# Kernel optimization log

Measured on AMD Instinct MI355X. Metric: run time of the kernel, lower is better.

Reference implementation:

```python
import jax, jax.numpy as jnp
import numpy as np


def _deform_conv2d(x, offset, weight, stride=(1, 1), pad=(1, 1), dilation=(1, 1)):
    # x: [B,C,H,W]; offset: [B, 2*Goff*kh*kw, oh, ow]; weight: [OC, C//Gw, kh, kw]
    B, C, H, W = x.shape
    OC, Cg, kh, kw = weight.shape
    Gw = C // Cg
    K = kh * kw
    sh, sw = stride
    ph, pw = pad
    dh, dw = dilation
    oh = (H + 2 * ph - (dh * (kh - 1) + 1)) // sh + 1
    ow = (W + 2 * pw - (dw * (kw - 1) + 1)) // sw + 1
    Goff = offset.shape[1] // (2 * K)
    # torchvision layout: per offset group, per kernel tap k, (dy, dx)
    off = offset.reshape(B, Goff, K, 2, oh, ow)
    ki = jnp.arange(K) // kw  # kernel row per tap
    kj = jnp.arange(K) % kw   # kernel col per tap
    base_y = jnp.arange(oh) * sh - ph
    base_x = jnp.arange(ow) * sw - pw
    gy = (base_y[None, :] + (ki * dh)[:, None]).astype(x.dtype)  # [K, oh]
    gx = (base_x[None, :] + (kj * dw)[:, None]).astype(x.dtype)  # [K, ow]
    py = off[:, :, :, 0] + gy[None, None, :, :, None]  # [B,Goff,K,oh,ow]
    px = off[:, :, :, 1] + gx[None, None, :, None, :]
    cpg = C // Goff  # channels per offset group
    py = jnp.repeat(py, cpg, axis=1)  # [B,C,K,oh,ow]
    px = jnp.repeat(px, cpg, axis=1)
    xf = x.reshape(B, C, H * W)
    y0 = jnp.floor(py)
    x0 = jnp.floor(px)
    ty = py - y0
    tx = px - x0
    y0i = y0.astype(jnp.int32)
    x0i = x0.astype(jnp.int32)

    def gather(cy, cx):
        valid = (cy >= 0) & (cy < H) & (cx >= 0) & (cx < W)
        idx = jnp.clip(cy, 0, H - 1) * W + jnp.clip(cx, 0, W - 1)
        v = jnp.take_along_axis(xf, idx.reshape(B, C, -1), axis=2).reshape(idx.shape)
        return jnp.where(valid, v, jnp.zeros((), x.dtype))

    # bilinear sample, zero padding outside image (matches torchvision)
    v = (gather(y0i, x0i) * (1 - ty) * (1 - tx)
         + gather(y0i, x0i + 1) * (1 - ty) * tx
         + gather(y0i + 1, x0i) * ty * (1 - tx)
         + gather(y0i + 1, x0i + 1) * ty * tx)  # [B,C,K,oh,ow]
    v = v.reshape(B, Gw, Cg, K, oh, ow)
    wg = weight.reshape(Gw, OC // Gw, Cg, K)
    out = jnp.einsum('bgckhw,gock->bgohw', v, wg)
    return out.reshape(B, OC, oh, ow)


def setup_inputs() -> dict:
    key = jax.random.key(0)
    k1, k2, k3 = jax.random.split(key, 3)
    x = jax.random.normal(k1, (8, 64, 56, 56), dtype=jnp.float32)
    offset = jax.random.normal(k2, (8, 18, 56, 56), dtype=jnp.float32)
    weight = jax.random.normal(k3, (64, 64, 3, 3), dtype=jnp.float32) * 0.05
    return {"input": x, "offset": offset, "weight": weight}


def reference(input, offset, weight):
    return _deform_conv2d(input, offset, weight, stride=(1, 1), pad=(1, 1), dilation=(1, 1))
```

## Files before the change

### kernel.cpp

```cpp
#include <hip/hip_runtime.h>
#include <hip/hip_fp16.h>


typedef _Float16 f16x8 __attribute__((ext_vector_type(8)));
typedef float    f32x4 __attribute__((ext_vector_type(4)));

namespace {
constexpr int Bn = 8, Cn = 64, Hn = 56, Wn = 56;
constexpr int Kk = 9, OCn = 64;
constexpr int NPIX = 56 * 56;
constexpr int CK   = Cn * Kk;
constexpr int TP   = 32;
constexpr int TXW  = 7;
constexpr int TILES = 98;
constexpr int XTILES = NPIX / 64;
constexpr int KSTEPS = CK / 32;
}

__device__ __forceinline__ __half2 u2h(unsigned u) {
    union { unsigned u; __half2 h; } x; x.u = u; return x.h;
}
__device__ __forceinline__ unsigned bcast_h(float f) {
    unsigned short hs = __half_as_ushort(__float2half(f));
    return (unsigned)hs * 0x10001u;
}
__device__ __forceinline__ void lds_barrier() {
    asm volatile("s_waitcnt lgkmcnt(0)" ::: "memory");
    __builtin_amdgcn_s_barrier();
}
__device__ __forceinline__ void gld16(uint4& d, const unsigned short* p) {
    asm volatile("global_load_dwordx4 %0, %1, off" : "=&v"(d) : "v"(p) : "memory");
}

__global__ __launch_bounds__(256) void prep_kernel(
    const float* __restrict__ x, const float* __restrict__ w,
    unsigned short* __restrict__ xh, unsigned short* __restrict__ wh2)
{
    const int tid = threadIdx.x;
    if (blockIdx.x >= 392) {
        const int i = (blockIdx.x - 392) * 256 + tid;
        if (i < OCn * CK) {
            const int j    = i & 7;
            const int lane = (i >> 3) & 63;
            const int rest = i >> 9;
            const int og   = rest / KSTEPS;
            const int oc   = og * 16 + (lane & 15);
            const int kglob = (rest % KSTEPS) * 32 + (lane >> 4) * 8 + j;
            const int tap = kglob >> 6;
            const int c   = kglob & 63;
            wh2[i] = __half_as_ushort(__float2half(w[oc * CK + c * Kk + tap]));
        }
        return;
    }
    __shared__ unsigned short lds[64][66];
    const int b  = blockIdx.x & 7;
    const int t0 = (blockIdx.x >> 3) * 64;
    const float* xb = x + (size_t)b * Cn * NPIX;
    {
        const int hw0 = (tid & 15) * 4;
        #pragma unroll
        for (int i = 0; i < 4; ++i) {
            const int c = (tid >> 4) + i * 16;
            const float4 v = *(const float4*)(xb + (size_t)c * NPIX + t0 + hw0);
            lds[hw0 + 0][c] = __half_as_ushort(__float2half(v.x));
            lds[hw0 + 1][c] = __half_as_ushort(__float2half(v.y));
            lds[hw0 + 2][c] = __half_as_ushort(__float2half(v.z));
            lds[hw0 + 3][c] = __half_as_ushort(__float2half(v.w));
        }
    }
    __syncthreads();
    {
        const int co = (tid & 7) * 8;
        #pragma unroll
        for (int i = 0; i < 2; ++i) {
            const int hw = (tid >> 3) + i * 32;
            unsigned short tmp[8] __attribute__((aligned(16)));
            #pragma unroll
            for (int j = 0; j < 8; ++j) tmp[j] = lds[hw][co + j];
            *(uint4*)(xh + ((size_t)b * NPIX + t0 + hw) * Cn + co) = *(const uint4*)tmp;
        }
    }
}

__global__ __launch_bounds__(256, 3) void deform_fused(
    const unsigned short* __restrict__ xh, const float* __restrict__ off,
    const unsigned short* __restrict__ wh2, float* __restrict__ out)
{
    __shared__ uint4 smpw[Kk * TP];
    __shared__ int4  smpa[Kk * TP];
    __shared__ __align__(16) uint4 vbuf[3][8 * TP];

    const int tid = threadIdx.x;
    const int b   = blockIdx.x & 7;
    const int t   = blockIdx.x >> 3;
    const int ox0 = (t % TXW) * 8;
    const int oy0 = (t / TXW) * 4;
    const unsigned short* xb = xh + (size_t)b * NPIX * Cn;
    const float* offb = off + (size_t)b * 18 * NPIX;

    for (int e = tid; e < Kk * TP; e += 256) {
        const int k  = e >> 5;
        const int px = e & 31;
        const int oy = oy0 + (px >> 3);
        const int ox = ox0 + (px & 7);
        const int p  = oy * Wn + ox;
        const int ki = k / 3, kj = k % 3;
        const float offy = offb[(size_t)(2 * k)     * NPIX + p];
        const float offx = offb[(size_t)(2 * k + 1) * NPIX + p];
        const float py  = offy + (float)(oy - 1 + ki);
        const float pxv = offx + (float)(ox - 1 + kj);
        const float y0f = floorf(py), x0f = floorf(pxv);
        const float ty = py - y0f, tx = pxv - x0f;
        const int y0 = (int)y0f, x0 = (int)x0f;
        const int y1 = y0 + 1, x1 = x0 + 1;
        const bool vy0 = (y0 >= 0) & (y0 < Hn);
        const bool vy1 = (y1 >= 0) & (y1 < Hn);
        const bool vx0 = (x0 >= 0) & (x0 < Wn);
        const bool vx1 = (x1 >= 0) & (x1 < Wn);
        const int cy0 = min(max(y0, 0), Hn - 1);
        const int cy1 = min(max(y1, 0), Hn - 1);
        const int cx0 = min(max(x0, 0), Wn - 1);
        const int cx1 = min(max(x1, 0), Wn - 1);
        uint4 wq;
        wq.x = bcast_h((vy0 && vx0) ? (1.f - ty) * (1.f - tx) : 0.f);
        wq.y = bcast_h((vy0 && vx1) ? (1.f - ty) * tx         : 0.f);
        wq.z = bcast_h((vy1 && vx0) ? ty * (1.f - tx)         : 0.f);
        wq.w = bcast_h((vy1 && vx1) ? ty * tx                 : 0.f);
        int4 av;
        av.x = (cy0 * Wn + cx0) * Cn;
        av.y = (cy0 * Wn + cx1) * Cn;
        av.z = (cy1 * Wn + cx0) * Cn;
        av.w = (cy1 * Wn + cx1) * Cn;
        smpw[e] = wq;
        smpa[e] = av;
    }
    lds_barrier();
    asm volatile("s_waitcnt vmcnt(0)" ::: "memory");

    const int oct = tid & 7;
    const int gpx = (tid >> 3) & 31;
    const int co  = oct * 8;

    const int lane = tid & 63;
    const int og   = tid >> 6;
    const int hi   = lane >> 4;
    const int lr   = lane & 15;
    const uint4* ab = (const uint4*)wh2 + (size_t)og * KSTEPS * 64 + lane;

    uint4 s0[2], s1[2], s2[2], s3[2], wqr[2];
    uint4 aF[2][2];
    f32x4 acc0 = {0.f, 0.f, 0.f, 0.f};
    f32x4 acc1 = {0.f, 0.f, 0.f, 0.f};

    auto stageC = [&](int k) {
        const int sl = k & 1;
        const int m  = k * TP + gpx;
        const int4 av = smpa[m];
        wqr[sl] = smpw[m];
        gld16(s0[sl], xb + av.x + co);
        gld16(s1[sl], xb + av.y + co);
        gld16(s2[sl], xb + av.z + co);
        gld16(s3[sl], xb + av.w + co);
    };
    auto loadA = [&](int k) {
        const int sl = k & 1;
        gld16(aF[sl][0], (const unsigned short*)(ab + (k * 2 + 0) * 64));
        gld16(aF[sl][1], (const unsigned short*)(ab + (k * 2 + 1) * 64));
    };
    auto blend = [&](int k) {
        const int sl = k & 1;
        const __half2 w00 = u2h(wqr[sl].x), w01 = u2h(wqr[sl].y);
        const __half2 w10 = u2h(wqr[sl].z), w11 = u2h(wqr[sl].w);
        uint4 res;
        unsigned* rp = (unsigned*)&res;
        #pragma unroll
        for (int q = 0; q < 4; ++q) {
            __half2 a = __hmul2(w00, u2h(((const unsigned*)&s0[sl])[q]));
            a = __hfma2(w01, u2h(((const unsigned*)&s1[sl])[q]), a);
            a = __hfma2(w10, u2h(((const unsigned*)&s2[sl])[q]), a);
            a = __hfma2(w11, u2h(((const unsigned*)&s3[sl])[q]), a);
            rp[q] = *(const unsigned*)&a;
        }
        vbuf[k % 3][oct * TP + gpx] = res;
    };
    auto mfma = [&](int k) {
        const int sl = k % 3;
        #pragma unroll
        for (int kl = 0; kl < 2; ++kl) {
            const int octr = kl * 4 + hi;
            union { uint4 u; f16x8 h; } a, b0, b1;
            a.u  = aF[k & 1][kl];
            b0.u = vbuf[sl][octr * TP + lr];
            b1.u = vbuf[sl][octr * TP + 16 + lr];
            acc0 = __builtin_amdgcn_mfma_f32_16x16x32_f16(a.h, b0.h, acc0, 0, 0, 0);
            acc1 = __builtin_amdgcn_mfma_f32_16x16x32_f16(a.h, b1.h, acc1, 0, 0, 0);
        }
    };

    stageC(0); stageC(1);
    loadA(0);
    asm volatile("s_waitcnt vmcnt(6)" ::: "memory");
    __builtin_amdgcn_sched_barrier(0);
    blend(0);
    lds_barrier();

    #pragma unroll
    for (int k = 0; k < Kk; ++k) {
        if (k < Kk - 2) stageC(k + 2);
        if (k < Kk - 1) loadA(k + 1);
        if (k < Kk - 2)      asm volatile("s_waitcnt vmcnt(6)" ::: "memory");
        else if (k == Kk - 2) asm volatile("s_waitcnt vmcnt(2)" ::: "memory");
        else                  asm volatile("s_waitcnt vmcnt(0)" ::: "memory");
        __builtin_amdgcn_sched_barrier(0);
        if (k < Kk - 1) blend(k + 1);
        mfma(k);
        lds_barrier();
    }

    const int p_lo = (oy0 + (lr >> 3)) * Wn + ox0 + (lr & 7);
    const int p_hi = (oy0 + 2 + (lr >> 3)) * Wn + ox0 + (lr & 7);
    float* ob = out + ((size_t)b * OCn + og * 16 + hi * 4) * NPIX;
    #pragma unroll
    for (int r = 0; r < 4; ++r) {
        ob[(size_t)r * NPIX + p_lo] = acc0[r];
        ob[(size_t)r * NPIX + p_hi] = acc1[r];
    }
}

extern "C" void kernel_launch(void* const* d_in, const int* in_sizes, int n_in,
                              void* d_out, int out_size, void* d_ws, size_t ws_size,
                              hipStream_t stream) {
    const float* x   = (const float*)d_in[0];
    const float* off = (const float*)d_in[1];
    const float* w   = (const float*)d_in[2];
    float* out = (float*)d_out;
    unsigned short* wh2 = (unsigned short*)d_ws;
    unsigned short* xh  = (unsigned short*)((char*)d_ws + 131072);

    hipLaunchKernelGGL(prep_kernel, dim3(392 + 144), dim3(256), 0, stream, x, w, xh, wh2);
    hipLaunchKernelGGL(deform_fused, dim3(Bn * TILES), dim3(256), 0, stream,
                       xh, off, wh2, out);
}
```

Before: 20.46 us.

## Stage input neighbourhood window in LDS and sample bilinear taps from shared memory

Each block first loads a 13x17-pixel, 64-channel fp16 window of the input around its 4x8 output tile into LDS. Bilinear corner samples whose coordinates fall inside the window are read from LDS, and those outside fall back to global loads. The hand-scheduled two-stage global-load pipeline with explicit vmcnt waits is replaced by a simpler blend-then-MFMA loop with a double-buffered vbuf. This cuts scattered global gathers but adds about 56KB of LDS per block, which may limit occupancy, and drops the overlap of gather latency with MFMA work.

```diff
diff --git a/kernel.cpp b/kernel.cpp
--- a/kernel.cpp
+++ b/kernel.cpp
@@ -15,6 +15,9 @@
 constexpr int TILES = 98;
 constexpr int XTILES = NPIX / 64;
 constexpr int KSTEPS = CK / 32;
+constexpr int WR = 13, WC = 17;
+constexpr int WSITES = WR * WC;
+constexpr int WU4 = WSITES * 8;
 }
 
 __device__ __forceinline__ __half2 u2h(unsigned u) {
@@ -27,9 +30,6 @@
 __device__ __forceinline__ void lds_barrier() {
     asm volatile("s_waitcnt lgkmcnt(0)" ::: "memory");
     __builtin_amdgcn_s_barrier();
-}
-__device__ __forceinline__ void gld16(uint4& d, const unsigned short* p) {
-    asm volatile("global_load_dwordx4 %0, %1, off" : "=&v"(d) : "v"(p) : "memory");
 }
 
 __global__ __launch_bounds__(256) void prep_kernel(
@@ -88,15 +88,30 @@
 {
     __shared__ uint4 smpw[Kk * TP];
     __shared__ int4  smpa[Kk * TP];
-    __shared__ __align__(16) uint4 vbuf[3][8 * TP];
+    __shared__ int4  smpl[Kk * TP];
+    __shared__ __align__(16) uint4 win[WU4];
+    __shared__ __align__(16) uint4 vbuf[2][8 * TP];
 
     const int tid = threadIdx.x;
     const int b   = blockIdx.x & 7;
     const int t   = blockIdx.x >> 3;
     const int ox0 = (t % TXW) * 8;
     const int oy0 = (t / TXW) * 4;
+    const int r0  = min(max(oy0 - 4, 0), Hn - WR);
+    const int c0  = min(max(ox0 - 4, 0), Wn - WC);
     const unsigned short* xb = xh + (size_t)b * NPIX * Cn;
     const float* offb = off + (size_t)b * 18 * NPIX;
+
+    uint4 st[7];
+    #pragma unroll
+    for (int it = 0; it < 7; ++it) {
+        const int u = tid + 256 * it;
+        if (u < WU4) {
+            const int i   = u / 136;
+            const int rem = u - i * 136;
+            st[it] = *(const uint4*)(xb + ((size_t)((r0 + i) * Wn + c0)) * Cn + rem * 8);
+        }
+    }
 
     for (int e = tid; e < Kk * TP; e += 256) {
         const int k  = e >> 5;
@@ -131,15 +146,28 @@
         av.y = (cy0 * Wn + cx1) * Cn;
         av.z = (cy1 * Wn + cx0) * Cn;
         av.w = (cy1 * Wn + cx1) * Cn;
+        const int i00y = cy0 - r0, i00x = cx0 - c0;
+        const int i11y = cy1 - r0, i11x = cx1 - c0;
+        int4 wl;
+        wl.x = ((unsigned)i00y < WR && (unsigned)i00x < WC) ? (i00y * WC + i00x) * 8 : -1;
+        wl.y = ((unsigned)i00y < WR && (unsigned)i11x < WC) ? (i00y * WC + i11x) * 8 : -1;
+        wl.z = ((unsigned)i11y < WR && (unsigned)i00x < WC) ? (i11y * WC + i00x) * 8 : -1;
+        wl.w = ((unsigned)i11y < WR && (unsigned)i11x < WC) ? (i11y * WC + i11x) * 8 : -1;
         smpw[e] = wq;
         smpa[e] = av;
-    }
-    lds_barrier();
-    asm volatile("s_waitcnt vmcnt(0)" ::: "memory");
+        smpl[e] = wl;
+    }
+
+    #pragma unroll
+    for (int it = 0; it < 7; ++it) {
+        const int u = tid + 256 * it;
+        if (u < WU4) win[u] = st[it];
+    }
+    __syncthreads();
 
     const int oct = tid & 7;
     const int gpx = (tid >> 3) & 31;
-    const int co  = oct * 8;
+    const int co8 = oct * 8;
 
     const int lane = tid & 63;
     const int og   = tid >> 6;
@@ -147,74 +175,61 @@
     const int lr   = lane & 15;
     const uint4* ab = (const uint4*)wh2 + (size_t)og * KSTEPS * 64 + lane;
 
-    uint4 s0[2], s1[2], s2[2], s3[2], wqr[2];
     uint4 aF[2][2];
     f32x4 acc0 = {0.f, 0.f, 0.f, 0.f};
     f32x4 acc1 = {0.f, 0.f, 0.f, 0.f};
 
-    auto stageC = [&](int k) {
-        const int sl = k & 1;
-        const int m  = k * TP + gpx;
-        const int4 av = smpa[m];
-        wqr[sl] = smpw[m];
-        gld16(s0[sl], xb + av.x + co);
-        gld16(s1[sl], xb + av.y + co);
-        gld16(s2[sl], xb + av.z + co);
-        gld16(s3[sl], xb + av.w + co);
-    };
     auto loadA = [&](int k) {
-        const int sl = k & 1;
-        gld16(aF[sl][0], (const unsigned short*)(ab + (k * 2 + 0) * 64));
-        gld16(aF[sl][1], (const unsigned short*)(ab + (k * 2 + 1) * 64));
+        aF[k & 1][0] = ab[(k * 2 + 0) * 64];
+        aF[k & 1][1] = ab[(k * 2 + 1) * 64];
     };
     auto blend = [&](int k) {
-        const int sl = k & 1;
-        const __half2 w00 = u2h(wqr[sl].x), w01 = u2h(wqr[sl].y);
-        const __half2 w10 = u2h(wqr[sl].z), w11 = u2h(wqr[sl].w);
+        const int m = k * TP + gpx;
+        const uint4 wq = smpw[m];
+        const int4  av = smpa[m];
+        const int4  wl = smpl[m];
+        uint4 v0 = win[(wl.x < 0 ? 0 : wl.x) + oct];
+        uint4 v1 = win[(wl.y < 0 ? 0 : wl.y) + oct];
+        uint4 v2 = win[(wl.z < 0 ? 0 : wl.z) + oct];
+        uint4 v3 = win[(wl.w < 0 ? 0 : wl.w) + oct];
+        if (wl.x < 0) v0 = *(const uint4*)(xb + av.x + co8);
+        if (wl.y < 0) v1 = *(const uint4*)(xb + av.y + co8);
+        if (wl.z < 0) v2 = *(const uint4*)(xb + av.z + co8);
+        if (wl.w < 0) v3 = *(const uint4*)(xb + av.w + co8);
+        const __half2 w00 = u2h(wq.x), w01 = u2h(wq.y);
+        const __half2 w10 = u2h(wq.z), w11 = u2h(wq.w);
         uint4 res;
         unsigned* rp = (unsigned*)&res;
         #pragma unroll
         for (int q = 0; q < 4; ++q) {
-            __half2 a = __hmul2(w00, u2h(((const unsigned*)&s0[sl])[q]));
-            a = __hfma2(w01, u2h(((const unsigned*)&s1[sl])[q]), a);
-            a = __hfma2(w10, u2h(((const unsigned*)&s2[sl])[q]), a);
-            a = __hfma2(w11, u2h(((const unsigned*)&s3[sl])[q]), a);
+            __half2 a = __hmul2(w00, u2h(((const unsigned*)&v0)[q]));
+            a = __hfma2(w01, u2h(((const unsigned*)&v1)[q]), a);
+            a = __hfma2(w10, u2h(((const unsigned*)&v2)[q]), a);
+            a = __hfma2(w11, u2h(((const unsigned*)&v3)[q]), a);
             rp[q] = *(const unsigned*)&a;
         }
-        vbuf[k % 3][oct * TP + gpx] = res;
+        vbuf[k & 1][oct * TP + gpx] = res;
     };
     auto mfma = [&](int k) {
-        const int sl = k % 3;
         #pragma unroll
         for (int kl = 0; kl < 2; ++kl) {
             const int octr = kl * 4 + hi;
             union { uint4 u; f16x8 h; } a, b0, b1;
             a.u  = aF[k & 1][kl];
-            b0.u = vbuf[sl][octr * TP + lr];
-            b1.u = vbuf[sl][octr * TP + 16 + lr];
+            b0.u = vbuf[k & 1][octr * TP + lr];
+            b1.u = vbuf[k & 1][octr * TP + 16 + lr];
             acc0 = __builtin_amdgcn_mfma_f32_16x16x32_f16(a.h, b0.h, acc0, 0, 0, 0);
             acc1 = __builtin_amdgcn_mfma_f32_16x16x32_f16(a.h, b1.h, acc1, 0, 0, 0);
         }
     };
 
-    stageC(0); stageC(1);
     loadA(0);
-    asm volatile("s_waitcnt vmcnt(6)" ::: "memory");
-    __builtin_amdgcn_sched_barrier(0);
-    blend(0);
-    lds_barrier();
-
     #pragma unroll
     for (int k = 0; k < Kk; ++k) {
-        if (k < Kk - 2) stageC(k + 2);
         if (k < Kk - 1) loadA(k + 1);
-        if (k < Kk - 2)      asm volatile("s_waitcnt vmcnt(6)" ::: "memory");
-        else if (k == Kk - 2) asm volatile("s_waitcnt vmcnt(2)" ::: "memory");
-        else                  asm volatile("s_waitcnt vmcnt(0)" ::: "memory");
-        __builtin_amdgcn_sched_barrier(0);
-        if (k < Kk - 1) blend(k + 1);
+        blend(k);
+        lds_barrier();
         mfma(k);
-        lds_barrier();
     }
 
     const int p_lo = (oy0 + (lr >> 3)) * Wn + ox0 + (lr & 7);
```

After: 31.23 us. +52.6%, slower.

## Warp-specialize deform kernel into gather/blend producer and MFMA consumer waves

Applied to the files above, without the earlier changes.

Splits the fused kernel into 6 waves per block: 2 producer waves gather the bilinear corner samples and blend them into the LDS ring buffer, and 4 consumer waves load weights and run MFMAs. The aim is to overlap gather latency with matrix work instead of having every wave do both serially. The cost is fewer waves doing the gathers (each handles two pixels), a larger block size that may lower occupancy under launch bounds, and barrier-coupled handoff between the roles.

```diff
diff --git a/kernel.cpp b/kernel.cpp
--- a/kernel.cpp
+++ b/kernel.cpp
@@ -15,6 +15,7 @@
 constexpr int TILES = 98;
 constexpr int XTILES = NPIX / 64;
 constexpr int KSTEPS = CK / 32;
+constexpr int NTHR = 384;
 }
 
 __device__ __forceinline__ __half2 u2h(unsigned u) {
@@ -82,7 +83,7 @@
     }
 }
 
-__global__ __launch_bounds__(256, 3) void deform_fused(
+__global__ __launch_bounds__(NTHR, 3) void deform_fused(
     const unsigned short* __restrict__ xh, const float* __restrict__ off,
     const unsigned short* __restrict__ wh2, float* __restrict__ out)
 {
@@ -98,7 +99,7 @@
     const unsigned short* xb = xh + (size_t)b * NPIX * Cn;
     const float* offb = off + (size_t)b * 18 * NPIX;
 
-    for (int e = tid; e < Kk * TP; e += 256) {
+    for (int e = tid; e < Kk * TP; e += NTHR) {
         const int k  = e >> 5;
         const int px = e & 31;
         const int oy = oy0 + (px >> 3);
@@ -137,93 +138,118 @@
     lds_barrier();
     asm volatile("s_waitcnt vmcnt(0)" ::: "memory");
 
-    const int oct = tid & 7;
-    const int gpx = (tid >> 3) & 31;
-    const int co  = oct * 8;
-
-    const int lane = tid & 63;
-    const int og   = tid >> 6;
-    const int hi   = lane >> 4;
-    const int lr   = lane & 15;
-    const uint4* ab = (const uint4*)wh2 + (size_t)og * KSTEPS * 64 + lane;
-
-    uint4 s0[2], s1[2], s2[2], s3[2], wqr[2];
-    uint4 aF[2][2];
-    f32x4 acc0 = {0.f, 0.f, 0.f, 0.f};
-    f32x4 acc1 = {0.f, 0.f, 0.f, 0.f};
-
-    auto stageC = [&](int k) {
-        const int sl = k & 1;
-        const int m  = k * TP + gpx;
-        const int4 av = smpa[m];
-        wqr[sl] = smpw[m];
-        gld16(s0[sl], xb + av.x + co);
-        gld16(s1[sl], xb + av.y + co);
-        gld16(s2[sl], xb + av.z + co);
-        gld16(s3[sl], xb + av.w + co);
-    };
-    auto loadA = [&](int k) {
-        const int sl = k & 1;
-        gld16(aF[sl][0], (const unsigned short*)(ab + (k * 2 + 0) * 64));
-        gld16(aF[sl][1], (const unsigned short*)(ab + (k * 2 + 1) * 64));
-    };
-    auto blend = [&](int k) {
-        const int sl = k & 1;
-        const __half2 w00 = u2h(wqr[sl].x), w01 = u2h(wqr[sl].y);
-        const __half2 w10 = u2h(wqr[sl].z), w11 = u2h(wqr[sl].w);
-        uint4 res;
-        unsigned* rp = (unsigned*)&res;
-        #pragma unroll
-        for (int q = 0; q < 4; ++q) {
-            __half2 a = __hmul2(w00, u2h(((const unsigned*)&s0[sl])[q]));
-            a = __hfma2(w01, u2h(((const unsigned*)&s1[sl])[q]), a);
-            a = __hfma2(w10, u2h(((const unsigned*)&s2[sl])[q]), a);
-            a = __hfma2(w11, u2h(((const unsigned*)&s3[sl])[q]), a);
-            rp[q] = *(const unsigned*)&a;
-        }
-        vbuf[k % 3][oct * TP + gpx] = res;
-    };
-    auto mfma = [&](int k) {
-        const int sl = k % 3;
-        #pragma unroll
-        for (int kl = 0; kl < 2; ++kl) {
-            const int octr = kl * 4 + hi;
-            union { uint4 u; f16x8 h; } a, b0, b1;
-            a.u  = aF[k & 1][kl];
-            b0.u = vbuf[sl][octr * TP + lr];
-            b1.u = vbuf[sl][octr * TP + 16 + lr];
-            acc0 = __builtin_amdgcn_mfma_f32_16x16x32_f16(a.h, b0.h, acc0, 0, 0, 0);
-            acc1 = __builtin_amdgcn_mfma_f32_16x16x32_f16(a.h, b1.h, acc1, 0, 0, 0);
-        }
-    };
-
-    stageC(0); stageC(1);
-    loadA(0);
-    asm volatile("s_waitcnt vmcnt(6)" ::: "memory");
-    __builtin_amdgcn_sched_barrier(0);
-    blend(0);
-    lds_barrier();
-
-    #pragma unroll
-    for (int k = 0; k < Kk; ++k) {
-        if (k < Kk - 2) stageC(k + 2);
-        if (k < Kk - 1) loadA(k + 1);
-        if (k < Kk - 2)      asm volatile("s_waitcnt vmcnt(6)" ::: "memory");
-        else if (k == Kk - 2) asm volatile("s_waitcnt vmcnt(2)" ::: "memory");
-        else                  asm volatile("s_waitcnt vmcnt(0)" ::: "memory");
+    const int wv = tid >> 6;
+
+    if (wv < 2) {
+        const int oct  = tid & 7;
+        const int gpx0 = (tid >> 3) & 15;
+        const int co   = oct * 8;
+
+        uint4 s0[2][2], s1[2][2], s2[2][2], s3[2][2], wqr[2][2];
+
+        auto stageC = [&](int k) {
+            const int sl = k & 1;
+            #pragma unroll
+            for (int u = 0; u < 2; ++u) {
+                const int m  = k * TP + gpx0 + u * 16;
+                const int4 av = smpa[m];
+                wqr[sl][u] = smpw[m];
+                gld16(s0[sl][u], xb + av.x + co);
+                gld16(s1[sl][u], xb + av.y + co);
+                gld16(s2[sl][u], xb + av.z + co);
+                gld16(s3[sl][u], xb + av.w + co);
+            }
+        };
+        auto blend = [&](int k) {
+            const int sl = k & 1;
+            #pragma unroll
+            for (int u = 0; u < 2; ++u) {
+                const __half2 w00 = u2h(wqr[sl][u].x), w01 = u2h(wqr[sl][u].y);
+                const __half2 w10 = u2h(wqr[sl][u].z), w11 = u2h(wqr[sl][u].w);
+                uint4 res;
+                unsigned* rp = (unsigned*)&res;
+                #pragma unroll
+                for (int q = 0; q < 4; ++q) {
+                    __half2 a = __hmul2(w00, u2h(((const unsigned*)&s0[sl][u])[q]));
+                    a = __hfma2(w01, u2h(((const unsigned*)&s1[sl][u])[q]), a);
+                    a = __hfma2(w10, u2h(((const unsigned*)&s2[sl][u])[q]), a);
+                    a = __hfma2(w11, u2h(((const unsigned*)&s3[sl][u])[q]), a);
+                    rp[q] = *(const unsigned*)&a;
+                }
+                vbuf[k % 3][oct * TP + gpx0 + u * 16] = res;
+            }
+        };
+
+        stageC(0); stageC(1);
+        asm volatile("s_waitcnt vmcnt(8)" ::: "memory");
         __builtin_amdgcn_sched_barrier(0);
-        if (k < Kk - 1) blend(k + 1);
-        mfma(k);
+        blend(0);
         lds_barrier();
-    }
-
-    const int p_lo = (oy0 + (lr >> 3)) * Wn + ox0 + (lr & 7);
-    const int p_hi = (oy0 + 2 + (lr >> 3)) * Wn + ox0 + (lr & 7);
-    float* ob = out + ((size_t)b * OCn + og * 16 + hi * 4) * NPIX;
-    #pragma unroll
-    for (int r = 0; r < 4; ++r) {
-        ob[(size_t)r * NPIX + p_lo] = acc0[r];
-        ob[(size_t)r * NPIX + p_hi] = acc1[r];
+
+        #pragma unroll
+        for (int k = 0; k < Kk; ++k) {
+            if (k < Kk - 2) {
+                stageC(k + 2);
+                asm volatile("s_waitcnt vmcnt(8)" ::: "memory");
+            } else if (k == Kk - 2) {
+                asm volatile("s_waitcnt vmcnt(0)" ::: "memory");
+            }
+            __builtin_amdgcn_sched_barrier(0);
+            if (k < Kk - 1) blend(k + 1);
+            lds_barrier();
+        }
+    } else {
+        const int lane = tid & 63;
+        const int og   = wv - 2;
+        const int hi   = lane >> 4;
+        const int lr   = lane & 15;
+        const uint4* ab = (const uint4*)wh2 + (size_t)og * KSTEPS * 64 + lane;
+
+        uint4 aF[2][2];
+        f32x4 acc0 = {0.f, 0.f, 0.f, 0.f};
+        f32x4 acc1 = {0.f, 0.f, 0.f, 0.f};
+
+        auto loadA = [&](int k) {
+            gld16(aF[k & 1][0], (const unsigned short*)(ab + (k * 2 + 0) * 64));
+            gld16(aF[k & 1][1], (const unsigned short*)(ab + (k * 2 + 1) * 64));
+        };
+        auto mfma = [&](int k) {
+            #pragma unroll
+            for (int kl = 0; kl < 2; ++kl) {
+                const int octr = kl * 4 + hi;
+                union { uint4 u; f16x8 h; } a, b0, b1;
+                a.u  = aF[k & 1][kl];
+                b0.u = vbuf[k % 3][octr * TP + lr];
+                b1.u = vbuf[k % 3][octr * TP + 16 + lr];
+                acc0 = __builtin_amdgcn_mfma_f32_16x16x32_f16(a.h, b0.h, acc0, 0, 0, 0);
+                acc1 = __builtin_amdgcn_mfma_f32_16x16x32_f16(a.h, b1.h, acc1, 0, 0, 0);
+            }
+        };
+
+        loadA(0);
+        lds_barrier();
+
+        #pragma unroll
+        for (int k = 0; k < Kk; ++k) {
+            if (k < Kk - 1) {
+                loadA(k + 1);
+                asm volatile("s_waitcnt vmcnt(2)" ::: "memory");
+            } else {
+                asm volatile("s_waitcnt vmcnt(0)" ::: "memory");
+            }
+            __builtin_amdgcn_sched_barrier(0);
+            mfma(k);
+            lds_barrier();
+        }
+
+        const int p_lo = (oy0 + (lr >> 3)) * Wn + ox0 + (lr & 7);
+        const int p_hi = (oy0 + 2 + (lr >> 3)) * Wn + ox0 + (lr & 7);
+        float* ob = out + ((size_t)b * OCn + og * 16 + hi * 4) * NPIX;
+        #pragma unroll
+        for (int r = 0; r < 4; ++r) {
+            ob[(size_t)r * NPIX + p_lo] = acc0[r];
+            ob[(size_t)r * NPIX + p_hi] = acc1[r];
+        }
     }
 }
 
@@ -238,6 +264,6 @@
     unsigned short* xh  = (unsigned short*)((char*)d_ws + 131072);
 
     hipLaunchKernelGGL(prep_kernel, dim3(392 + 144), dim3(256), 0, stream, x, w, xh, wh2);
-    hipLaunchKernelGGL(deform_fused, dim3(Bn * TILES), dim3(256), 0, stream,
+    hipLaunchKernelGGL(deform_fused, dim3(Bn * TILES), dim3(NTHR), 0, stream,
                        xh, off, wh2, out);
 }
```

After: 21.70 us. +6.1%, slower.
